# Performance work log

Measured on AMD Instinct MI355X. Metric: run time of the kernel, lower is better.

## Reference

```python
import jax, jax.numpy as jnp
import numpy as np

N, E, F, H, O, G = 50000, 800000, 50, 512, 121, 20
EPS = 1e-5


def _lin(k, out_f, in_f):
    return jax.random.normal(k, (out_f, in_f), jnp.float32) / np.sqrt(in_f)


def setup_inputs() -> dict:
    key = jax.random.key(0)
    ks = jax.random.split(key, 32)
    inp = {
        "x": jax.random.normal(ks[0], (N, F), jnp.float32),
        "edge_index": jax.random.randint(ks[1], (2, E), 0, N, jnp.int64 if jax.config.jax_enable_x64 else jnp.int32),
        "batch": jnp.sort(jax.random.randint(ks[2], (N,), 0, G, jnp.int32)),
    }
    dims = [(F, H), (H, H), (H, H), (H, H), (H, O)]
    ki = 3
    for i, (fi, fo) in enumerate(dims, start=1):
        inp[f"W{i}l"] = _lin(ks[ki], fo, fi); ki += 1
        inp[f"W{i}r"] = _lin(ks[ki], fo, fi); ki += 1
        inp[f"b{i}"] = jnp.zeros((fo,), jnp.float32)
    for i in range(1, 5):
        inp[f"g{i}"] = jnp.ones((H,), jnp.float32)    # GraphNorm weight
        inp[f"bn{i}"] = jnp.zeros((H,), jnp.float32)  # GraphNorm bias
        inp[f"a{i}"] = jnp.ones((H,), jnp.float32)    # GraphNorm mean_scale
    return inp


def _sage(x, src, dst, inv_deg, Wl, Wr, b):
    # mean aggregation of neighbor messages x[src] at dst, then two linears
    agg = jax.ops.segment_sum(x[src], dst, num_segments=N) * inv_deg  # [N, Fin]
    return agg @ Wl.T + x @ Wr.T + b


def _gnorm(x, batch, inv_sz, w, b, alpha):
    mean = jax.ops.segment_sum(x, batch, num_segments=G) * inv_sz  # [G, C]
    out = x - alpha * mean[batch]
    var = jax.ops.segment_sum(out * out, batch, num_segments=G) * inv_sz
    return out * jax.lax.rsqrt(var[batch] + EPS) * w + b


def reference(x, edge_index, batch,
              W1l, W1r, b1, W2l, W2r, b2, W3l, W3r, b3, W4l, W4r, b4, W5l, W5r, b5,
              g1, bn1, a1, g2, bn2, a2, g3, bn3, a3, g4, bn4, a4):
    src, dst = edge_index[0], edge_index[1]
    deg = jax.ops.segment_sum(jnp.ones((E,), jnp.float32), dst, num_segments=N)
    inv_deg = (1.0 / jnp.maximum(deg, 1.0))[:, None]
    sz = jax.ops.segment_sum(jnp.ones((N,), jnp.float32), batch, num_segments=G)
    inv_sz = (1.0 / jnp.maximum(sz, 1.0))[:, None]

    h = _sage(x, src, dst, inv_deg, W1l, W1r, b1)
    h = jax.nn.relu(_gnorm(h, batch, inv_sz, g1, bn1, a1))  # dropout=identity (eval)
    h = _sage(h, src, dst, inv_deg, W2l, W2r, b2)
    h = jax.nn.relu(_gnorm(h, batch, inv_sz, g2, bn2, a2))
    h = _sage(h, src, dst, inv_deg, W3l, W3r, b3)
    h = jax.nn.relu(_gnorm(h, batch, inv_sz, g3, bn3, a3))
    h = _sage(h, src, dst, inv_deg, W4l, W4r, b4)
    h = jax.nn.relu(_gnorm(h, batch, inv_sz, g4, bn4, a4))
    return _sage(h, src, dst, inv_deg, W5l, W5r, b5)
```

## Files before the change

kernel.cpp:

```cpp
#include <hip/hip_runtime.h>
#include <cstddef>
#include <cstdint>

#define N_NODES 50000
#define N_EDGES 800000
#define F_IN 50
#define K1PAD 64
#define H_DIM 512
#define O_DIM 121
#define N_GROUPS 20
#define EPSV 1e-5f
#define M_PAD 50048
#define M_TILES 391

#define SCAN_BLK 256
#define SCAN_NBLK ((N_NODES + SCAN_BLK - 1) / SCAN_BLK)
#define WALL_EL 1769472
#define XB_EL (M_PAD * K1PAD)

typedef unsigned short u16;
typedef __attribute__((ext_vector_type(8))) short short8;
typedef __attribute__((ext_vector_type(8))) unsigned short u16x8;
typedef __attribute__((ext_vector_type(4))) float f32x4;

__device__ __forceinline__ float b2f(u16 u) {
  union { unsigned int i; float f; } v; v.i = ((unsigned int)u) << 16; return v.f;
}
__device__ __forceinline__ u16 f2b(float f) {
  union { float f; unsigned int i; } v; v.f = f;
  unsigned int x = v.i;
  return (u16)((x + 0x7fffu + ((x >> 16) & 1u)) >> 16);
}

__device__ __forceinline__ void gl_lds16(const void* g, void* l) {
  __builtin_amdgcn_global_load_lds(
      (__attribute__((address_space(1))) void*)(g),
      (__attribute__((address_space(3))) void*)(l), 16, 0, 0);
}


__global__ void k_deg(const int* __restrict__ dst, int* __restrict__ deg) {
  int e = blockIdx.x * blockDim.x + threadIdx.x;
  if (e < N_EDGES) atomicAdd(&deg[dst[e]], 1);
}

__global__ void k_scan1(const int* __restrict__ deg, int* __restrict__ off,
                        int* __restrict__ bsum) {
  __shared__ int buf[SCAN_BLK];
  int gid = blockIdx.x * SCAN_BLK + threadIdx.x;
  buf[threadIdx.x] = (gid < N_NODES) ? deg[gid] : 0;
  __syncthreads();
  for (int d = 1; d < SCAN_BLK; d <<= 1) {
    int t = (threadIdx.x >= d) ? buf[threadIdx.x - d] : 0;
    __syncthreads();
    buf[threadIdx.x] += t;
    __syncthreads();
  }
  if (gid < N_NODES) off[gid + 1] = buf[threadIdx.x];
  if (threadIdx.x == SCAN_BLK - 1) bsum[blockIdx.x] = buf[threadIdx.x];
}

__global__ void k_scan2_gbounds(int* __restrict__ bsum, const int* __restrict__ batch,
                                int* __restrict__ gstart, float* __restrict__ inv_sz) {
  int t = threadIdx.x;
  if (blockIdx.x == 0) {
    __shared__ int buf[256];
    buf[t] = (t < SCAN_NBLK) ? bsum[t] : 0;
    __syncthreads();
    for (int d = 1; d < 256; d <<= 1) {
      int v = (t >= d) ? buf[t - d] : 0;
      __syncthreads();
      buf[t] += v;
      __syncthreads();
    }
    if (t < SCAN_NBLK) bsum[t] = buf[t];
  } else {
    if (t <= N_GROUPS) {
      int lo = 0, hi = N_NODES;
      while (lo < hi) {
        int mid = (lo + hi) >> 1;
        if (batch[mid] < t) lo = mid + 1; else hi = mid;
      }
      gstart[t] = lo;
    }
    __syncthreads();
    if (t < N_GROUPS) {
      int sz = gstart[t + 1] - gstart[t];
      inv_sz[t] = 1.0f / (float)max(sz, 1);
    }
  }
}

__global__ void k_scan3prep(int* __restrict__ off, const int* __restrict__ bsum,
                            const int* __restrict__ deg, float* __restrict__ inv_deg,
                            int* __restrict__ cursor) {
  int gid = blockIdx.x * SCAN_BLK + threadIdx.x;
  if (gid < N_NODES) {
    int add = (blockIdx.x > 0) ? bsum[blockIdx.x - 1] : 0;
    int v = off[gid + 1] + add;
    off[gid + 1] = v;
    if (gid + 1 < N_NODES) cursor[gid + 1] = v;
    inv_deg[gid] = 1.0f / (float)max(deg[gid], 1);
  }
  if (gid == 0) { off[0] = 0; cursor[0] = 0; }
}

__global__ void k_scatter(const int* __restrict__ src, const int* __restrict__ dst,
                          int* __restrict__ cursor, int* __restrict__ csr_src) {
  int e = blockIdx.x * blockDim.x + threadIdx.x;
  if (e < N_EDGES) {
    int p = atomicAdd(&cursor[dst[e]], 1);
    csr_src[p] = src[e];
  }
}

struct WcSrc { const float* p[10]; };
__global__ void k_convert_all(const float* __restrict__ x, WcSrc s,
                              u16* __restrict__ xb, u16* __restrict__ wall) {
  int idx = blockIdx.x * blockDim.x + threadIdx.x;
  if (idx < XB_EL) {
    int r = idx >> 6, c = idx & (K1PAD - 1);
    float v = (r < N_NODES && c < F_IN) ? x[r * F_IN + c] : 0.f;
    xb[idx] = f2b(v);
    return;
  }
  idx -= XB_EL;
  if (idx >= WALL_EL) return;
  const int seg_start[10] = {0, 32768, 65536, 327680, 589824, 851968,
                             1114112, 1376256, 1638400, 1703936};
  const int jr[10]  = {512, 512, 512, 512, 512, 512, 512, 512, 121, 121};
  const int kin[10] = {50, 50, 512, 512, 512, 512, 512, 512, 512, 512};
  const int ksh[10] = {6, 6, 9, 9, 9, 9, 9, 9, 9, 9};
  int sgi = 0;
#pragma unroll
  for (int t = 1; t < 10; ++t)
    if (idx >= seg_start[t]) sgi = t;
  int local = idx - seg_start[sgi];
  int j = local >> ksh[sgi];
  int k = local & ((1 << ksh[sgi]) - 1);
  float v = (j < jr[sgi] && k < kin[sgi]) ? s.p[sgi][j * kin[sgi] + k] : 0.f;
  wall[idx] = f2b(v);
}


__global__ void k_agg_small(const u16* __restrict__ xb, const int* __restrict__ off,
                            const int* __restrict__ srcs, const float* __restrict__ inv_deg,
                            u16* __restrict__ agg) {
  int n = blockIdx.x;
  int f = threadIdx.x;
  int b = off[n], e = off[n + 1];
  float s = 0.f;
  for (int i = b; i < e; ++i) s += b2f(xb[(size_t)srcs[i] * K1PAD + f]);
  agg[(size_t)n * K1PAD + f] = f2b(s * inv_deg[n]);
}

__global__ __launch_bounds__(512) void k_agg512(
    const u16* __restrict__ h, const int* __restrict__ off,
    const int* __restrict__ srcs, const float* __restrict__ inv_deg,
    u16* __restrict__ agg) {
  __shared__ float part[4][64][8];
  int slot = threadIdx.y >> 1;
  int sub = threadIdx.y & 1;
  int n = blockIdx.x * 4 + slot;
  int t = threadIdx.x;
  float a[8] = {0.f, 0.f, 0.f, 0.f, 0.f, 0.f, 0.f, 0.f};
  if (n < N_NODES) {
    int b = off[n], e = off[n + 1];
    int half = (e - b + 1) >> 1;
    int lo = b + sub * half;
    int hi = min(lo + half, e);
    int i = lo;
    for (; i + 4 <= hi; i += 4) {
      u16x8 v0 = ((const u16x8*)(h + (size_t)srcs[i + 0] * H_DIM))[t];
      u16x8 v1 = ((const u16x8*)(h + (size_t)srcs[i + 1] * H_DIM))[t];
      u16x8 v2 = ((const u16x8*)(h + (size_t)srcs[i + 2] * H_DIM))[t];
      u16x8 v3 = ((const u16x8*)(h + (size_t)srcs[i + 3] * H_DIM))[t];
#pragma unroll
      for (int j = 0; j < 8; ++j)
        a[j] += (b2f(v0[j]) + b2f(v1[j])) + (b2f(v2[j]) + b2f(v3[j]));
    }
    for (; i < hi; ++i) {
      u16x8 v0 = ((const u16x8*)(h + (size_t)srcs[i] * H_DIM))[t];
#pragma unroll
      for (int j = 0; j < 8; ++j) a[j] += b2f(v0[j]);
    }
  }
  if (sub == 1) {
#pragma unroll
    for (int j = 0; j < 8; ++j) part[slot][t][j] = a[j];
  }
  __syncthreads();
  if (sub == 0 && n < N_NODES) {
    float w = inv_deg[n];
    u16x8 r;
#pragma unroll
    for (int j = 0; j < 8; ++j) r[j] = f2b((a[j] + part[slot][t][j]) * w);
    ((u16x8*)(agg + (size_t)n * H_DIM))[t] = r;
  }
}

__global__ __launch_bounds__(256) void k_agg_final(
    const u16* __restrict__ Plb, const float* __restrict__ Prf,
    const int* __restrict__ off, const int* __restrict__ srcs,
    const float* __restrict__ inv_deg, const float* __restrict__ bias,
    float* __restrict__ out) {
  int n = blockIdx.x * 8 + (threadIdx.x >> 5);
  if (n >= N_NODES) return;
  int l = threadIdx.x & 31;
  int c0 = l * 4;
  int b = off[n], e = off[n + 1];
  float a0 = 0.f, a1 = 0.f, a2 = 0.f, a3 = 0.f;
  int i = b;
  for (; i + 2 <= e; i += 2) {
    ushort4 v0 = ((const ushort4*)(Plb + (size_t)srcs[i] * 128))[l];
    ushort4 v1 = ((const ushort4*)(Plb + (size_t)srcs[i + 1] * 128))[l];
    a0 += b2f(v0.x) + b2f(v1.x); a1 += b2f(v0.y) + b2f(v1.y);
    a2 += b2f(v0.z) + b2f(v1.z); a3 += b2f(v0.w) + b2f(v1.w);
  }
  if (i < e) {
    ushort4 v0 = ((const ushort4*)(Plb + (size_t)srcs[i] * 128))[l];
    a0 += b2f(v0.x); a1 += b2f(v0.y); a2 += b2f(v0.z); a3 += b2f(v0.w);
  }
  float w = inv_deg[n];
  float4 pr = ((const float4*)(Prf + (size_t)n * 128))[l];
  float r0 = a0 * w + pr.x, r1 = a1 * w + pr.y;
  float r2 = a2 * w + pr.z, r3 = a3 * w + pr.w;
  size_t ob = (size_t)n * O_DIM;
  if (c0 + 0 < O_DIM) out[ob + c0 + 0] = r0 + bias[c0 + 0];
  if (c0 + 1 < O_DIM) out[ob + c0 + 1] = r1 + bias[c0 + 1];
  if (c0 + 2 < O_DIM) out[ob + c0 + 2] = r2 + bias[c0 + 2];
  if (c0 + 3 < O_DIM) out[ob + c0 + 3] = r3 + bias[c0 + 3];
}


#define TM 128
#define TK 32

template <int JB, bool DUAL, int OUTMODE>
__global__ __launch_bounds__(256, 4) void k_gemm_mfma(
    const u16* __restrict__ A, const u16* __restrict__ X,
    const u16* __restrict__ Wl, const u16* __restrict__ Wr,
    const float* __restrict__ bias, void* __restrict__ C0,
    void* __restrict__ C1, const int* __restrict__ batch,
    float* __restrict__ ssum, float* __restrict__ ssq, int K) {
  __shared__ u16 As[TM * TK];
  __shared__ u16 Ls[TM * TK];
  __shared__ u16 Xs[DUAL ? TM * TK : 1];
  __shared__ u16 Rs[DUAL ? TM * TK : 1];

  int id = blockIdx.x;
  const int nfull = (M_TILES >> 3) * 8 * JB;
  int m_t, j_t;
  if (id < nfull) {
    m_t = (id / (8 * JB)) * 8 + (id & 7);
    j_t = (id >> 3) & (JB - 1);
  } else {
    int rem = id - nfull;
    const int nrem = M_TILES & 7;
    m_t = (M_TILES & ~7) + rem % nrem;
    j_t = rem / nrem;
  }
  int m0 = m_t * TM;
  int j0 = j_t * 128;

  int tid = threadIdx.x;
  int lane = tid & 63;
  int wave = tid >> 6;
  int quad = lane >> 4;
  int lr = lane & 15;
  int wm = (wave & 1) * 64;
  int wn = (wave >> 1) * 64;

  f32x4 acc[4][4] = {};

  int sr = tid >> 2;
  int sc = (tid & 3) * 8;
  size_t moff0 = (size_t)(m0 + sr) * K + sc;
  size_t moff1 = moff0 + (size_t)64 * K;
  size_t joff0 = (size_t)(j0 + sr) * K + sc;
  size_t joff1 = joff0 + (size_t)64 * K;
  const int dofs = tid * 8;

  for (int k0 = 0; k0 < K; k0 += TK) {
    __syncthreads();
    gl_lds16(A + moff0 + k0, As + dofs);
    gl_lds16(A + moff1 + k0, As + 2048 + dofs);
    gl_lds16(Wl + joff0 + k0, Ls + dofs);
    gl_lds16(Wl + joff1 + k0, Ls + 2048 + dofs);
    if constexpr (DUAL) {
      gl_lds16(X + moff0 + k0, Xs + dofs);
      gl_lds16(X + moff1 + k0, Xs + 2048 + dofs);
      gl_lds16(Wr + joff0 + k0, Rs + dofs);
      gl_lds16(Wr + joff1 + k0, Rs + 2048 + dofs);
    }
    __syncthreads();
    {
      short8 af[4], lf[4];
#pragma unroll
      for (int t = 0; t < 4; ++t) {
        af[t] = *(const short8*)(As + (wm + t * 16 + lr) * TK + quad * 8);
        lf[t] = *(const short8*)(Ls + (wn + t * 16 + lr) * TK + quad * 8);
      }
#pragma unroll
      for (int ti = 0; ti < 4; ++ti)
#pragma unroll
        for (int tj = 0; tj < 4; ++tj)
          acc[ti][tj] = __builtin_amdgcn_mfma_f32_16x16x32_bf16(
              af[ti], lf[tj], acc[ti][tj], 0, 0, 0);
    }
    if constexpr (DUAL) {
      short8 xf[4], rf[4];
#pragma unroll
      for (int t = 0; t < 4; ++t) {
        xf[t] = *(const short8*)(Xs + (wm + t * 16 + lr) * TK + quad * 8);
        rf[t] = *(const short8*)(Rs + (wn + t * 16 + lr) * TK + quad * 8);
      }
#pragma unroll
      for (int ti = 0; ti < 4; ++ti)
#pragma unroll
        for (int tj = 0; tj < 4; ++tj)
          acc[ti][tj] = __builtin_amdgcn_mfma_f32_16x16x32_bf16(
              xf[ti], rf[tj], acc[ti][tj], 0, 0, 0);
    }
  }

  if constexpr (OUTMODE == 0) {
    int glo = batch[m0];
    int lastrow = m0 + TM - 1;
    bool fast = (lastrow < N_NODES) && (batch[lastrow] == glo);
#pragma unroll
    for (int tj = 0; tj < 4; ++tj) {
      int gcol = j0 + wn + tj * 16 + lr;
      float bv = bias[gcol];
      float s = 0.f, q = 0.f;
#pragma unroll
      for (int ti = 0; ti < 4; ++ti) {
        f32x4 v = acc[ti][tj];
        int rbase = m0 + wm + ti * 16 + quad * 4;
        if (fast) {
#pragma unroll
          for (int r = 0; r < 4; ++r) {
            float val = v[r] + bv;
            ((u16*)C0)[(size_t)(rbase + r) * H_DIM + gcol] = f2b(val);
            s += val; q += val * val;
          }
        } else {
          if (rbase + 3 < N_NODES && batch[rbase] == batch[rbase + 3]) {
            float s4 = 0.f, q4 = 0.f;
#pragma unroll
            for (int r = 0; r < 4; ++r) {
              float val = v[r] + bv;
              ((u16*)C0)[(size_t)(rbase + r) * H_DIM + gcol] = f2b(val);
              s4 += val; q4 += val * val;
            }
            int g = batch[rbase];
            atomicAdd(&ssum[g * H_DIM + gcol], s4);
            atomicAdd(&ssq[g * H_DIM + gcol], q4);
          } else {
#pragma unroll
            for (int r = 0; r < 4; ++r) {
              int grow = rbase + r;
              if (grow < N_NODES) {
                float val = v[r] + bv;
                ((u16*)C0)[(size_t)grow * H_DIM + gcol] = f2b(val);
                int g = batch[grow];
                atomicAdd(&ssum[g * H_DIM + gcol], val);
                atomicAdd(&ssq[g * H_DIM + gcol], val * val);
              }
            }
          }
        }
      }
      if (fast) {
        s += __shfl_xor(s, 16); s += __shfl_xor(s, 32);
        q += __shfl_xor(q, 16); q += __shfl_xor(q, 32);
        if (quad == 0) {
          atomicAdd(&ssum[glo * H_DIM + gcol], s);
          atomicAdd(&ssq[glo * H_DIM + gcol], q);
        }
      }
    }
  } else {
#pragma unroll
    for (int tj = 0; tj < 4; ++tj) {
      int gcol = j0 + wn + tj * 16 + lr;
#pragma unroll
      for (int ti = 0; ti < 4; ++ti) {
        f32x4 v = acc[ti][tj];
#pragma unroll
        for (int r = 0; r < 4; ++r) {
          int grow = m0 + wm + ti * 16 + quad * 4 + r;
          if (gcol < 128)
            ((u16*)C0)[(size_t)grow * 128 + gcol] = f2b(v[r]);
          else
            ((float*)C1)[(size_t)grow * 128 + (gcol - 128)] = v[r];
        }
      }
    }
  }
}


__global__ void k_precomp(const float* __restrict__ ssum, const float* __restrict__ ssq,
                          const float* __restrict__ inv_sz, const float* __restrict__ gw,
                          const float* __restrict__ gb, const float* __restrict__ alpha,
                          float* __restrict__ S, float* __restrict__ T) {
  int idx = blockIdx.x * blockDim.x + threadIdx.x;
  if (idx >= N_GROUPS * H_DIM) return;
  int g = idx >> 9;
  int c = idx & (H_DIM - 1);
  float is = inv_sz[g];
  float m = ssum[idx] * is;
  float a = alpha[c];
  float var = fmaxf(ssq[idx] * is - a * (2.f - a) * m * m, 0.f);
  float inv = rsqrtf(var + EPSV);
  float sc = inv * gw[c];
  S[idx] = sc;
  T[idx] = gb[c] - a * m * sc;
}

__global__ void k_apply(u16* __restrict__ h, const int* __restrict__ batch,
                        const float* __restrict__ S, const float* __restrict__ T) {
  int tid = blockIdx.x * blockDim.x + threadIdx.x;
  if (tid >= N_NODES * (H_DIM / 8)) return;
  int n = tid >> 6;
  int c0 = (tid & 63) << 3;
  int g = batch[n];
  u16x8 hv = *(const u16x8*)(h + (size_t)n * H_DIM + c0);
  u16x8 out;
#pragma unroll
  for (int j = 0; j < 8; ++j) {
    int f = c0 + j;
    float y = b2f(hv[j]) * S[g * H_DIM + f] + T[g * H_DIM + f];
    out[j] = f2b(fmaxf(y, 0.f));
  }
  *(u16x8*)(h + (size_t)n * H_DIM + c0) = out;
}


extern "C" void kernel_launch(void* const* d_in, const int* in_sizes, int n_in,
                              void* d_out, int out_size, void* d_ws, size_t ws_size,
                              hipStream_t stream) {
  const float* x = (const float*)d_in[0];
  const int* edge = (const int*)d_in[1];
  const int* batch = (const int*)d_in[2];
  const float *Wl[5], *Wr[5], *bb[5];
  for (int i = 0; i < 5; ++i) {
    Wl[i] = (const float*)d_in[3 + 3 * i];
    Wr[i] = (const float*)d_in[4 + 3 * i];
    bb[i] = (const float*)d_in[5 + 3 * i];
  }
  const float *gamma[4], *beta[4], *alpha[4];
  for (int i = 0; i < 4; ++i) {
    gamma[i] = (const float*)d_in[18 + 3 * i];
    beta[i]  = (const float*)d_in[19 + 3 * i];
    alpha[i] = (const float*)d_in[20 + 3 * i];
  }
  const int* srcv = edge;
  const int* dstv = edge + N_EDGES;

  char* base = (char*)d_ws;
  size_t off = 0;
  auto carve = [&](size_t bytes) -> char* {
    char* p = base + off;
    off = (off + bytes + 255) & ~(size_t)255;
    return p;
  };
  int* deg       = (int*)carve((size_t)N_NODES * 4);
  float* inv_deg = (float*)carve((size_t)N_NODES * 4);
  int* csr_off   = (int*)carve((size_t)(N_NODES + 1) * 4);
  int* cursor    = (int*)carve((size_t)N_NODES * 4);
  int* csr_src   = (int*)carve((size_t)N_EDGES * 4);
  int* bsum      = (int*)carve((size_t)SCAN_NBLK * 4);
  int* gstart    = (int*)carve((size_t)(N_GROUPS + 1) * 4);
  float* inv_sz  = (float*)carve((size_t)N_GROUPS * 4);
  float* stats   = (float*)carve((size_t)4 * 2 * N_GROUPS * H_DIM * 4);
  float* Sbuf    = (float*)carve((size_t)N_GROUPS * H_DIM * 4);
  float* Tbuf    = (float*)carve((size_t)N_GROUPS * H_DIM * 4);
  u16* xb        = (u16*)carve((size_t)XB_EL * 2);
  u16* aggx      = (u16*)carve((size_t)XB_EL * 2);
  u16* h0        = (u16*)carve((size_t)M_PAD * H_DIM * 2);
  u16* h1        = (u16*)carve((size_t)M_PAD * H_DIM * 2);
  u16* h2        = (u16*)carve((size_t)M_PAD * H_DIM * 2);
  u16* wall      = (u16*)carve((size_t)WALL_EL * 2);
  (void)ws_size; (void)in_sizes; (void)n_in; (void)out_size;

  u16* w1lb = wall;
  u16* w1rb = wall + 32768;
  u16* w2lb = wall + 65536;
  u16* w2rb = wall + 327680;
  u16* w3lb = wall + 589824;
  u16* w3rb = wall + 851968;
  u16* w4lb = wall + 1114112;
  u16* w4rb = wall + 1376256;
  u16* w5cat = wall + 1638400;

  u16* Plb = h1;
  float* Prf = (float*)((char*)h1 + (size_t)M_PAD * 128 * 2);

  hipMemsetAsync(deg, 0, (size_t)N_NODES * 4, stream);
  k_deg<<<(N_EDGES + 255) / 256, 256, 0, stream>>>(dstv, deg);
  k_scan1<<<SCAN_NBLK, SCAN_BLK, 0, stream>>>(deg, csr_off, bsum);
  k_scan2_gbounds<<<2, 256, 0, stream>>>(bsum, batch, gstart, inv_sz);
  k_scan3prep<<<SCAN_NBLK, SCAN_BLK, 0, stream>>>(csr_off, bsum, deg, inv_deg, cursor);
  k_scatter<<<(N_EDGES + 255) / 256, 256, 0, stream>>>(srcv, dstv, cursor, csr_src);

  WcSrc ws_src;
  ws_src.p[0] = Wl[0]; ws_src.p[1] = Wr[0];
  ws_src.p[2] = Wl[1]; ws_src.p[3] = Wr[1];
  ws_src.p[4] = Wl[2]; ws_src.p[5] = Wr[2];
  ws_src.p[6] = Wl[3]; ws_src.p[7] = Wr[3];
  ws_src.p[8] = Wl[4]; ws_src.p[9] = Wr[4];
  k_convert_all<<<(XB_EL + WALL_EL + 255) / 256, 256, 0, stream>>>(x, ws_src, xb, wall);

  hipMemsetAsync(stats, 0, (size_t)4 * 2 * N_GROUPS * H_DIM * 4, stream);

  const int nblk_main = M_TILES * 4;
  const int nblk_l5   = M_TILES * 2;
  dim3 aggblk(64, 8);
  int aggrid = (N_NODES + 3) / 4;

  auto norm = [&](u16* h, int l) {
    float* ss = stats + (size_t)l * 2 * N_GROUPS * H_DIM;
    float* sq = ss + N_GROUPS * H_DIM;
    k_precomp<<<(N_GROUPS * H_DIM + 255) / 256, 256, 0, stream>>>(
        ss, sq, inv_sz, gamma[l], beta[l], alpha[l], Sbuf, Tbuf);
    k_apply<<<(N_NODES * (H_DIM / 8) + 255) / 256, 256, 0, stream>>>(
        h, batch, Sbuf, Tbuf);
  };
  auto stat_ptr = [&](int l) { return stats + (size_t)l * 2 * N_GROUPS * H_DIM; };

  k_agg_small<<<N_NODES, 64, 0, stream>>>(xb, csr_off, csr_src, inv_deg, aggx);
  k_gemm_mfma<4, true, 0><<<nblk_main, 256, 0, stream>>>(
      aggx, xb, w1lb, w1rb, bb[0], h0, nullptr, batch,
      stat_ptr(0), stat_ptr(0) + N_GROUPS * H_DIM, K1PAD);
  norm(h0, 0);

  k_agg512<<<aggrid, aggblk, 0, stream>>>(h0, csr_off, csr_src, inv_deg, h1);
  k_gemm_mfma<4, true, 0><<<nblk_main, 256, 0, stream>>>(
      h1, h0, w2lb, w2rb, bb[1], h2, nullptr, batch,
      stat_ptr(1), stat_ptr(1) + N_GROUPS * H_DIM, H_DIM);
  norm(h2, 1);

  k_agg512<<<aggrid, aggblk, 0, stream>>>(h2, csr_off, csr_src, inv_deg, h0);
  k_gemm_mfma<4, true, 0><<<nblk_main, 256, 0, stream>>>(
      h0, h2, w3lb, w3rb, bb[2], h1, nullptr, batch,
      stat_ptr(2), stat_ptr(2) + N_GROUPS * H_DIM, H_DIM);
  norm(h1, 2);

  k_agg512<<<aggrid, aggblk, 0, stream>>>(h1, csr_off, csr_src, inv_deg, h2);
  k_gemm_mfma<4, true, 0><<<nblk_main, 256, 0, stream>>>(
      h2, h1, w4lb, w4rb, bb[3], h0, nullptr, batch,
      stat_ptr(3), stat_ptr(3) + N_GROUPS * H_DIM, H_DIM);
  norm(h0, 3);

  k_gemm_mfma<2, false, 1><<<nblk_l5, 256, 0, stream>>>(
      h0, nullptr, w5cat, nullptr, nullptr, Plb, Prf, nullptr, nullptr, nullptr, H_DIM);
  k_agg_final<<<(N_NODES + 7) / 8, 256, 0, stream>>>(
      Plb, Prf, csr_off, csr_src, inv_deg, bb[4], (float*)d_out);
}
```

Measured before the change: 1.075 ms.

## Fuse GraphNorm apply into stats and last GEMM, merge conversion with layer-1 aggregation

Removes the separate per-layer precompute kernel by computing the norm scale/shift inline in k_apply, which now writes out-of-place. For layer 4 the normalize+ReLU is folded into the A-tile load of the final GEMM. The x/weight bf16 conversion and the first-layer neighbor aggregation are merged into one launch, with aggregation reading fp32 x directly. Nontemporal stores are added to the aggregation and apply outputs. Together these cut kernel launches and one full read-modify-write pass over the hidden state. The cost is extra per-tile loads and ALU work in the last GEMM and out-of-place buffer juggling.

```diff
diff --git a/kernel.cpp b/kernel.cpp
--- a/kernel.cpp
+++ b/kernel.cpp
@@ -17,6 +17,7 @@
 #define SCAN_NBLK ((N_NODES + SCAN_BLK - 1) / SCAN_BLK)
 #define WALL_EL 1769472
 #define XB_EL (M_PAD * K1PAD)
+#define CONV_BLKS ((XB_EL + WALL_EL) / 256)
 
 typedef unsigned short u16;
 typedef __attribute__((ext_vector_type(8))) short short8;
@@ -115,43 +116,44 @@
 }
 
 struct WcSrc { const float* p[10]; };
-__global__ void k_convert_all(const float* __restrict__ x, WcSrc s,
-                              u16* __restrict__ xb, u16* __restrict__ wall) {
-  int idx = blockIdx.x * blockDim.x + threadIdx.x;
-  if (idx < XB_EL) {
-    int r = idx >> 6, c = idx & (K1PAD - 1);
-    float v = (r < N_NODES && c < F_IN) ? x[r * F_IN + c] : 0.f;
-    xb[idx] = f2b(v);
-    return;
-  }
-  idx -= XB_EL;
-  if (idx >= WALL_EL) return;
-  const int seg_start[10] = {0, 32768, 65536, 327680, 589824, 851968,
-                             1114112, 1376256, 1638400, 1703936};
-  const int jr[10]  = {512, 512, 512, 512, 512, 512, 512, 512, 121, 121};
-  const int kin[10] = {50, 50, 512, 512, 512, 512, 512, 512, 512, 512};
-  const int ksh[10] = {6, 6, 9, 9, 9, 9, 9, 9, 9, 9};
-  int sgi = 0;
-#pragma unroll
-  for (int t = 1; t < 10; ++t)
-    if (idx >= seg_start[t]) sgi = t;
-  int local = idx - seg_start[sgi];
-  int j = local >> ksh[sgi];
-  int k = local & ((1 << ksh[sgi]) - 1);
-  float v = (j < jr[sgi] && k < kin[sgi]) ? s.p[sgi][j * kin[sgi] + k] : 0.f;
-  wall[idx] = f2b(v);
-}
-
-
-__global__ void k_agg_small(const u16* __restrict__ xb, const int* __restrict__ off,
-                            const int* __restrict__ srcs, const float* __restrict__ inv_deg,
-                            u16* __restrict__ agg) {
-  int n = blockIdx.x;
-  int f = threadIdx.x;
-  int b = off[n], e = off[n + 1];
-  float s = 0.f;
-  for (int i = b; i < e; ++i) s += b2f(xb[(size_t)srcs[i] * K1PAD + f]);
-  agg[(size_t)n * K1PAD + f] = f2b(s * inv_deg[n]);
+__global__ void k_conv_agg(const float* __restrict__ x, WcSrc s,
+                           u16* __restrict__ xb, u16* __restrict__ wall,
+                           const int* __restrict__ off, const int* __restrict__ srcs,
+                           const float* __restrict__ inv_deg, u16* __restrict__ aggx) {
+  if (blockIdx.x < CONV_BLKS) {
+    int idx = blockIdx.x * 256 + threadIdx.x;
+    if (idx < XB_EL) {
+      int r = idx >> 6, c = idx & (K1PAD - 1);
+      float v = (r < N_NODES && c < F_IN) ? x[r * F_IN + c] : 0.f;
+      xb[idx] = f2b(v);
+      return;
+    }
+    idx -= XB_EL;
+    const int seg_start[10] = {0, 32768, 65536, 327680, 589824, 851968,
+                               1114112, 1376256, 1638400, 1703936};
+    const int jr[10]  = {512, 512, 512, 512, 512, 512, 512, 512, 121, 121};
+    const int kin[10] = {50, 50, 512, 512, 512, 512, 512, 512, 512, 512};
+    const int ksh[10] = {6, 6, 9, 9, 9, 9, 9, 9, 9, 9};
+    int sgi = 0;
+#pragma unroll
+    for (int t = 1; t < 10; ++t)
+      if (idx >= seg_start[t]) sgi = t;
+    int local = idx - seg_start[sgi];
+    int j = local >> ksh[sgi];
+    int k = local & ((1 << ksh[sgi]) - 1);
+    float v = (j < jr[sgi] && k < kin[sgi]) ? s.p[sgi][j * kin[sgi] + k] : 0.f;
+    wall[idx] = f2b(v);
+  } else {
+    int aid = blockIdx.x - CONV_BLKS;
+    int n = aid * 4 + (threadIdx.x >> 6);
+    if (n >= N_NODES) return;
+    int f = threadIdx.x & 63;
+    int b = off[n], e = off[n + 1];
+    float sacc = 0.f;
+    if (f < F_IN)
+      for (int i = b; i < e; ++i) sacc += x[(size_t)srcs[i] * F_IN + f];
+    aggx[(size_t)n * K1PAD + f] = f2b(sacc * inv_deg[n]);
+  }
 }
 
 __global__ __launch_bounds__(512) void k_agg512(
@@ -195,7 +197,7 @@
     u16x8 r;
 #pragma unroll
     for (int j = 0; j < 8; ++j) r[j] = f2b((a[j] + part[slot][t][j]) * w);
-    ((u16x8*)(agg + (size_t)n * H_DIM))[t] = r;
+    __builtin_nontemporal_store(r, (u16x8*)(agg + (size_t)n * H_DIM) + t);
   }
 }
 
@@ -236,13 +238,14 @@
 #define TM 128
 #define TK 32
 
-template <int JB, bool DUAL, int OUTMODE>
+template <int JB, bool DUAL, int OUTMODE, bool NORM>
 __global__ __launch_bounds__(256, 4) void k_gemm_mfma(
     const u16* __restrict__ A, const u16* __restrict__ X,
     const u16* __restrict__ Wl, const u16* __restrict__ Wr,
     const float* __restrict__ bias, void* __restrict__ C0,
     void* __restrict__ C1, const int* __restrict__ batch,
-    float* __restrict__ ssum, float* __restrict__ ssq, int K) {
+    float* __restrict__ ssum, float* __restrict__ ssq,
+    const float* __restrict__ Sn, const float* __restrict__ Tn, int K) {
   __shared__ u16 As[TM * TK];
   __shared__ u16 Ls[TM * TK];
   __shared__ u16 Xs[DUAL ? TM * TK : 1];
@@ -281,10 +284,40 @@
   size_t joff1 = joff0 + (size_t)64 * K;
   const int dofs = tid * 8;
 
+  int g0 = 0, g1 = 0;
+  if constexpr (NORM) {
+    int r0 = m0 + sr, r1 = m0 + sr + 64;
+    g0 = (r0 < N_NODES) ? batch[r0] : 0;
+    g1 = (r1 < N_NODES) ? batch[r1] : 0;
+  }
+
   for (int k0 = 0; k0 < K; k0 += TK) {
     __syncthreads();
-    gl_lds16(A + moff0 + k0, As + dofs);
-    gl_lds16(A + moff1 + k0, As + 2048 + dofs);
+    if constexpr (!NORM) {
+      gl_lds16(A + moff0 + k0, As + dofs);
+      gl_lds16(A + moff1 + k0, As + 2048 + dofs);
+    } else {
+      u16x8 ra = *(const u16x8*)(A + moff0 + k0);
+      u16x8 rb = *(const u16x8*)(A + moff1 + k0);
+      f32x4 s0a = *(const f32x4*)(Sn + g0 * H_DIM + k0 + sc);
+      f32x4 s0b = *(const f32x4*)(Sn + g0 * H_DIM + k0 + sc + 4);
+      f32x4 t0a = *(const f32x4*)(Tn + g0 * H_DIM + k0 + sc);
+      f32x4 t0b = *(const f32x4*)(Tn + g0 * H_DIM + k0 + sc + 4);
+      f32x4 s1a = *(const f32x4*)(Sn + g1 * H_DIM + k0 + sc);
+      f32x4 s1b = *(const f32x4*)(Sn + g1 * H_DIM + k0 + sc + 4);
+      f32x4 t1a = *(const f32x4*)(Tn + g1 * H_DIM + k0 + sc);
+      f32x4 t1b = *(const f32x4*)(Tn + g1 * H_DIM + k0 + sc + 4);
+      u16x8 wa, wb;
+#pragma unroll
+      for (int j = 0; j < 4; ++j) {
+        wa[j]     = f2b(fmaxf(b2f(ra[j])     * s0a[j] + t0a[j], 0.f));
+        wa[j + 4] = f2b(fmaxf(b2f(ra[j + 4]) * s0b[j] + t0b[j], 0.f));
+        wb[j]     = f2b(fmaxf(b2f(rb[j])     * s1a[j] + t1a[j], 0.f));
+        wb[j + 4] = f2b(fmaxf(b2f(rb[j + 4]) * s1b[j] + t1b[j], 0.f));
+      }
+      *(u16x8*)(As + dofs) = wa;
+      *(u16x8*)(As + 2048 + dofs) = wb;
+    }
     gl_lds16(Wl + joff0 + k0, Ls + dofs);
     gl_lds16(Wl + joff1 + k0, Ls + 2048 + dofs);
     if constexpr (DUAL) {
@@ -400,6 +433,35 @@
   }
 }
 
+
+__global__ void k_apply(const u16* __restrict__ hr, u16* __restrict__ hn,
+                        const int* __restrict__ batch,
+                        const float* __restrict__ ssum, const float* __restrict__ ssq,
+                        const float* __restrict__ inv_sz, const float* __restrict__ gw,
+                        const float* __restrict__ gb, const float* __restrict__ alpha) {
+  int tid = blockIdx.x * blockDim.x + threadIdx.x;
+  int n = tid >> 5;
+  if (n >= N_NODES) return;
+  int c0 = (tid & 31) << 4;
+  int g = batch[n];
+  float is = inv_sz[g];
+  u16x8 h0v = *(const u16x8*)(hr + (size_t)n * H_DIM + c0);
+  u16x8 h1v = *(const u16x8*)(hr + (size_t)n * H_DIM + c0 + 8);
+  u16x8 o0, o1;
+#pragma unroll
+  for (int j = 0; j < 16; ++j) {
+    int c = c0 + j;
+    float m = ssum[g * H_DIM + c] * is;
+    float a = alpha[c];
+    float var = fmaxf(ssq[g * H_DIM + c] * is - a * (2.f - a) * m * m, 0.f);
+    float sc = rsqrtf(var + EPSV) * gw[c];
+    float xv = (j < 8) ? b2f(h0v[j]) : b2f(h1v[j - 8]);
+    float y = fmaxf((xv - a * m) * sc + gb[c], 0.f);
+    if (j < 8) o0[j] = f2b(y); else o1[j - 8] = f2b(y);
+  }
+  __builtin_nontemporal_store(o0, (u16x8*)(hn + (size_t)n * H_DIM + c0));
+  __builtin_nontemporal_store(o1, (u16x8*)(hn + (size_t)n * H_DIM + c0 + 8));
+}
 
 __global__ void k_precomp(const float* __restrict__ ssum, const float* __restrict__ ssq,
                           const float* __restrict__ inv_sz, const float* __restrict__ gw,
@@ -417,24 +479,6 @@
   float sc = inv * gw[c];
   S[idx] = sc;
   T[idx] = gb[c] - a * m * sc;
-}
-
-__global__ void k_apply(u16* __restrict__ h, const int* __restrict__ batch,
-                        const float* __restrict__ S, const float* __restrict__ T) {
-  int tid = blockIdx.x * blockDim.x + threadIdx.x;
-  if (tid >= N_NODES * (H_DIM / 8)) return;
-  int n = tid >> 6;
-  int c0 = (tid & 63) << 3;
-  int g = batch[n];
-  u16x8 hv = *(const u16x8*)(h + (size_t)n * H_DIM + c0);
-  u16x8 out;
-#pragma unroll
-  for (int j = 0; j < 8; ++j) {
-    int f = c0 + j;
-    float y = b2f(hv[j]) * S[g * H_DIM + f] + T[g * H_DIM + f];
-    out[j] = f2b(fmaxf(y, 0.f));
-  }
-  *(u16x8*)(h + (size_t)n * H_DIM + c0) = out;
 }
 
 
@@ -504,6 +548,7 @@
   k_scan2_gbounds<<<2, 256, 0, stream>>>(bsum, batch, gstart, inv_sz);
   k_scan3prep<<<SCAN_NBLK, SCAN_BLK, 0, stream>>>(csr_off, bsum, deg, inv_deg, cursor);
   k_scatter<<<(N_EDGES + 255) / 256, 256, 0, stream>>>(srcv, dstv, cursor, csr_src);
+  hipMemsetAsync(stats, 0, (size_t)4 * 2 * N_GROUPS * H_DIM * 4, stream);
 
   WcSrc ws_src;
   ws_src.p[0] = Wl[0]; ws_src.p[1] = Wr[0];
@@ -511,51 +556,43 @@
   ws_src.p[4] = Wl[2]; ws_src.p[5] = Wr[2];
   ws_src.p[6] = Wl[3]; ws_src.p[7] = Wr[3];
   ws_src.p[8] = Wl[4]; ws_src.p[9] = Wr[4];
-  k_convert_all<<<(XB_EL + WALL_EL + 255) / 256, 256, 0, stream>>>(x, ws_src, xb, wall);
-
-  hipMemsetAsync(stats, 0, (size_t)4 * 2 * N_GROUPS * H_DIM * 4, stream);
+  k_conv_agg<<<CONV_BLKS + (N_NODES + 3) / 4, 256, 0, stream>>>(
+      x, ws_src, xb, wall, csr_off, csr_src, inv_deg, aggx);
 
   const int nblk_main = M_TILES * 4;
   const int nblk_l5   = M_TILES * 2;
   dim3 aggblk(64, 8);
   int aggrid = (N_NODES + 3) / 4;
-
-  auto norm = [&](u16* h, int l) {
-    float* ss = stats + (size_t)l * 2 * N_GROUPS * H_DIM;
-    float* sq = ss + N_GROUPS * H_DIM;
-    k_precomp<<<(N_GROUPS * H_DIM + 255) / 256, 256, 0, stream>>>(
-        ss, sq, inv_sz, gamma[l], beta[l], alpha[l], Sbuf, Tbuf);
-    k_apply<<<(N_NODES * (H_DIM / 8) + 255) / 256, 256, 0, stream>>>(
-        h, batch, Sbuf, Tbuf);
+  int apgrid = (N_NODES * 32 + 255) / 256;
+
+  auto stat_ptr = [&](int l) { return stats + (size_t)l * 2 * N_GROUPS * H_DIM; };
+  auto apply = [&](int l) {
+    k_apply<<<apgrid, 256, 0, stream>>>(
+        h0, h1, batch, stat_ptr(l), stat_ptr(l) + N_GROUPS * H_DIM,
+        inv_sz, gamma[l], beta[l], alpha[l]);
   };
-  auto stat_ptr = [&](int l) { return stats + (size_t)l * 2 * N_GROUPS * H_DIM; };
-
-  k_agg_small<<<N_NODES, 64, 0, stream>>>(xb, csr_off, csr_src, inv_deg, aggx);
-  k_gemm_mfma<4, true, 0><<<nblk_main, 256, 0, stream>>>(
+
+  k_gemm_mfma<4, true, 0, false><<<nblk_main, 256, 0, stream>>>(
       aggx, xb, w1lb, w1rb, bb[0], h0, nullptr, batch,
-      stat_ptr(0), stat_ptr(0) + N_GROUPS * H_DIM, K1PAD);
-  norm(h0, 0);
-
-  k_agg512<<<aggrid, aggblk, 0, stream>>>(h0, csr_off, csr_src, inv_deg, h1);
-  k_gemm_mfma<4, true, 0><<<nblk_main, 256, 0, stream>>>(
-      h1, h0, w2lb, w2rb, bb[1], h2, nullptr, batch,
-      stat_ptr(1), stat_ptr(1) + N_GROUPS * H_DIM, H_DIM);
-  norm(h2, 1);
-
-  k_agg512<<<aggrid, aggblk, 0, stream>>>(h2, csr_off, csr_src, inv_deg, h0);
-  k_gemm_mfma<4, true, 0><<<nblk_main, 256, 0, stream>>>(
-      h0, h2, w3lb, w3rb, bb[2], h1, nullptr, batch,
-      stat_ptr(2), stat_ptr(2) + N_GROUPS * H_DIM, H_DIM);
-  norm(h1, 2);
-
-  k_agg512<<<aggrid, aggblk, 0, stream>>>(h1, csr_off, csr_src, inv_deg, h2);
-  k_gemm_mfma<4, true, 0><<<nblk_main, 256, 0, stream>>>(
-      h2, h1, w4lb, w4rb, bb[3], h0, nullptr, batch,
-      stat_ptr(3), stat_ptr(3) + N_GROUPS * H_DIM, H_DIM);
-  norm(h0, 3);
-
-  k_gemm_mfma<2, false, 1><<<nblk_l5, 256, 0, stream>>>(
-      h0, nullptr, w5cat, nullptr, nullptr, Plb, Prf, nullptr, nullptr, nullptr, H_DIM);
+      stat_ptr(0), stat_ptr(0) + N_GROUPS * H_DIM, nullptr, nullptr, K1PAD);
+  apply(0);
+
+  const u16* wls[3] = {w2lb, w3lb, w4lb};
+  const u16* wrs[3] = {w2rb, w3rb, w4rb};
+  for (int l = 1; l <= 3; ++l) {
+    k_agg512<<<aggrid, aggblk, 0, stream>>>(h1, csr_off, csr_src, inv_deg, h2);
+    k_gemm_mfma<4, true, 0, false><<<nblk_main, 256, 0, stream>>>(
+        h2, h1, wls[l - 1], wrs[l - 1], bb[l], h0, nullptr, batch,
+        stat_ptr(l), stat_ptr(l) + N_GROUPS * H_DIM, nullptr, nullptr, H_DIM);
+    if (l < 3) apply(l);
+  }
+
+  k_precomp<<<(N_GROUPS * H_DIM + 255) / 256, 256, 0, stream>>>(
+      stat_ptr(3), stat_ptr(3) + N_GROUPS * H_DIM, inv_sz,
+      gamma[3], beta[3], alpha[3], Sbuf, Tbuf);
+  k_gemm_mfma<2, false, 1, true><<<nblk_l5, 256, 0, stream>>>(
+      h0, nullptr, w5cat, nullptr, nullptr, Plb, Prf, batch,
+      nullptr, nullptr, Sbuf, Tbuf, H_DIM);
   k_agg_final<<<(N_NODES + 7) / 8, 256, 0, stream>>>(
       Plb, Prf, csr_off, csr_src, inv_deg, bb[4], (float*)d_out);
 }
```

Measured after the change: 1.182 ms. 1.1x slower.
